# Optimization experiments

Hardware: AMD Instinct MI355X
Metric: run time of the kernel (lower is better)

Reference implementation:

```python
import jax, jax.numpy as jnp
import numpy as np

N = 20000   # nodes
E = 320000  # directed edges (before self-loops)
D = 64      # input_dim
H = 10      # GAT heads
HD = H * D  # 640
NEG_SLOPE = 0.2


def setup_inputs() -> dict:
    key = jax.random.key(0)
    ks = jax.random.split(key, 10)
    return {
        "x": jax.random.normal(ks[0], (N, D), jnp.float32),
        "W_gat": jax.random.normal(ks[1], (D, HD), jnp.float32) / np.sqrt(D).astype(np.float32),
        "att_src": jax.random.normal(ks[2], (H, D), jnp.float32) / np.sqrt(D).astype(np.float32),
        "att_dst": jax.random.normal(ks[3], (H, D), jnp.float32) / np.sqrt(D).astype(np.float32),
        "b_gat": jnp.zeros((HD,), jnp.float32),
        "W_gcn": jax.random.normal(ks[4], (HD, HD), jnp.float32) / np.sqrt(HD).astype(np.float32),
        "b_gcn": jnp.zeros((HD,), jnp.float32),
        "W1": jax.random.normal(ks[5], (2 * HD, 1500), jnp.float32) / np.sqrt(2 * HD).astype(np.float32),
        "b1": jnp.zeros((1500,), jnp.float32),
        "W2": jax.random.normal(ks[6], (1500, 10), jnp.float32) / np.sqrt(1500).astype(np.float32),
        "b2": jnp.zeros((10,), jnp.float32),
        "edge_index": jax.random.randint(ks[7], (2, E), 0, N, dtype=jnp.int64),
    }


def _forward(x, W_gat, att_src, att_dst, b_gat, W_gcn, b_gcn, W1, b1, W2, b2, edge_index):
    n = x.shape[0]
    # add self-loops (PyG default for both GATConv and GCNConv)
    loop = jnp.arange(n, dtype=edge_index.dtype)
    ei = jnp.concatenate([edge_index, jnp.stack([loop, loop])], axis=1)
    src, dst = ei[0], ei[1]

    # ---- GATConv(D -> D, heads=H, concat) ----
    xl = (x @ W_gat).reshape(n, H, D)                      # [N,H,D]
    a_src = jnp.einsum('nhd,hd->nh', xl, att_src)          # [N,H]
    a_dst = jnp.einsum('nhd,hd->nh', xl, att_dst)          # [N,H]
    alpha = jax.nn.leaky_relu(a_src[src] + a_dst[dst], NEG_SLOPE)  # [E',H]
    m = jax.ops.segment_max(alpha, dst, num_segments=n)    # segment softmax over incoming edges
    ex = jnp.exp(alpha - m[dst])
    den = jax.ops.segment_sum(ex, dst, num_segments=n)
    w = ex / (den[dst] + 1e-16)                            # [E',H]
    msg = xl[src] * w[:, :, None]                          # [E',H,D]
    x1 = jax.ops.segment_sum(msg, dst, num_segments=n).reshape(n, HD) + b_gat
    x1 = jax.nn.relu(x1)

    # ---- GCNConv(HD -> HD), symmetric norm with self-loops ----
    deg = jax.ops.segment_sum(jnp.ones(ei.shape[1], x.dtype), dst, num_segments=n)
    dinv = jnp.where(deg > 0, jax.lax.rsqrt(deg), 0.0)
    norm = dinv[src] * dinv[dst]                           # [E']
    xw = x1 @ W_gcn                                        # [N,HD]
    x2 = jax.ops.segment_sum(xw[src] * norm[:, None], dst, num_segments=n) + b_gcn
    x2 = jax.nn.relu(x2)

    # ---- global max/mean pool (batch=None -> single graph) + MLP head ----
    pooled = jnp.concatenate([x2.max(axis=0, keepdims=True),
                              x2.mean(axis=0, keepdims=True)], axis=1)  # [1, 2*HD]
    h = jax.nn.relu(pooled @ W1 + b1)
    # dropout is identity in eval mode
    return h @ W2 + b2                                     # [1, 10]


def reference(x, W_gat, att_src, att_dst, b_gat, W_gcn, b_gcn, W1, b1, W2, b2, edge_index):
    return _forward(x, W_gat, att_src, att_dst, b_gat, W_gcn, b_gcn, W1, b1, W2, b2, edge_index)
```

## Files before the change

### kernel.cpp

```cpp
#include <hip/hip_runtime.h>
#include <hip/hip_bf16.h>
#include <math.h>

#define NN 20000
#define DD 64
#define HH 10
#define HDIM 640
#define NEG 0.2f
#define H1 1500
#define BKK 128

typedef _Float16 half8 __attribute__((ext_vector_type(8)));
typedef _Float16 half4v __attribute__((ext_vector_type(4)));
typedef float f32x4 __attribute__((ext_vector_type(4)));

__global__ __launch_bounds__(256) void k_cvtB(const float* __restrict__ Wgcn,
                                              const float* __restrict__ Wg,
                                              _Float16* __restrict__ Wbt,
                                              _Float16* __restrict__ WgT)
{
    __shared__ float t[32][33];
    const int bx = blockIdx.x;
    int by = blockIdx.y;
    const float* W; _Float16* WT; int rows, cols;
    if (by < 20) { W = Wgcn; WT = Wbt; rows = HDIM; cols = HDIM; }
    else         { W = Wg;   WT = WgT; rows = DD;   cols = HDIM; by -= 20; }
    const int lx = threadIdx.x & 31, ly = threadIdx.x >> 5;
    #pragma unroll
    for (int i = ly; i < 32; i += 8)
        t[i][lx] = W[(size_t)(by * 32 + i) * cols + bx * 32 + lx];
    __syncthreads();
    #pragma unroll
    for (int j = ly; j < 32; j += 8)
        WT[(size_t)(bx * 32 + j) * rows + by * 32 + lx] = (_Float16)t[lx][j];
}

__global__ __launch_bounds__(256) void k_gemm1(
    const float* __restrict__ x, const _Float16* __restrict__ WgT,
    const float* __restrict__ att_s, const float* __restrict__ att_d,
    _Float16* __restrict__ xl, float* __restrict__ aST, float* __restrict__ aDT)
{
    __shared__ _Float16 As[128][72];
    __shared__ _Float16 Bs[64][72];
    const int tid = threadIdx.x;
    const int m0 = blockIdx.x * 128;
    const int h  = blockIdx.y;
    const int n0 = h * 64;

    {
        const int row = tid >> 1, ch = (tid & 1) * 32;
        const int gr = m0 + row;
        if (gr < NN) {
            const float* xp = &x[(size_t)gr * DD + ch];
            #pragma unroll
            for (int i = 0; i < 8; ++i) {
                const float4 v = *(const float4*)&xp[i * 4];
                half4v o = {(_Float16)v.x, (_Float16)v.y, (_Float16)v.z, (_Float16)v.w};
                *(half4v*)&As[row][ch + i * 4] = o;
            }
        } else {
            const half8 z = {0, 0, 0, 0, 0, 0, 0, 0};
            #pragma unroll
            for (int i = 0; i < 4; ++i) *(half8*)&As[row][ch + i * 8] = z;
        }
    }
    {
        const int row = tid >> 2, part = (tid & 3) * 16;
        const _Float16* wp = &WgT[(size_t)(n0 + row) * DD + part];
        *(half8*)&Bs[row][part]     = *(const half8*)&wp[0];
        *(half8*)&Bs[row][part + 8] = *(const half8*)&wp[8];
    }
    __syncthreads();

    const int lane = tid & 63, wave = tid >> 6;
    const int l15 = lane & 15, quad = lane >> 4;
    f32x4 acc[2][4];
    #pragma unroll
    for (int r = 0; r < 2; ++r)
        #pragma unroll
        for (int c = 0; c < 4; ++c) acc[r][c] = (f32x4){0.f, 0.f, 0.f, 0.f};

    #pragma unroll
    for (int ks = 0; ks < 2; ++ks) {
        const half8 a0 = *(const half8*)&As[wave * 32 + l15][ks * 32 + quad * 8];
        const half8 a1 = *(const half8*)&As[wave * 32 + 16 + l15][ks * 32 + quad * 8];
        #pragma unroll
        for (int c = 0; c < 4; ++c) {
            const half8 b = *(const half8*)&Bs[c * 16 + l15][ks * 32 + quad * 8];
            acc[0][c] = __builtin_amdgcn_mfma_f32_16x16x32_f16(a0, b, acc[0][c], 0, 0, 0);
            acc[1][c] = __builtin_amdgcn_mfma_f32_16x16x32_f16(a1, b, acc[1][c], 0, 0, 0);
        }
    }

    float asv[4], adv[4];
    #pragma unroll
    for (int c = 0; c < 4; ++c) {
        asv[c] = att_s[h * DD + c * 16 + l15];
        adv[c] = att_d[h * DD + c * 16 + l15];
    }
    #pragma unroll
    for (int r = 0; r < 2; ++r) {
        float ps[4] = {0.f, 0.f, 0.f, 0.f}, pd[4] = {0.f, 0.f, 0.f, 0.f};
        #pragma unroll
        for (int c = 0; c < 4; ++c)
            #pragma unroll
            for (int g = 0; g < 4; ++g) {
                ps[g] = fmaf(acc[r][c][g], asv[c], ps[g]);
                pd[g] = fmaf(acc[r][c][g], adv[c], pd[g]);
            }
        #pragma unroll
        for (int m = 1; m <= 8; m <<= 1)
            #pragma unroll
            for (int g = 0; g < 4; ++g) {
                ps[g] += __shfl_xor(ps[g], m);
                pd[g] += __shfl_xor(pd[g], m);
            }
        #pragma unroll
        for (int c = 0; c < 4; ++c)
            #pragma unroll
            for (int g = 0; g < 4; ++g) {
                const int row = m0 + wave * 32 + r * 16 + quad * 4 + g;
                if (row < NN)
                    xl[(size_t)row * HDIM + n0 + c * 16 + l15] = (_Float16)acc[r][c][g];
            }
        if (l15 == 0)
            #pragma unroll
            for (int g = 0; g < 4; ++g) {
                const int row = m0 + wave * 32 + r * 16 + quad * 4 + g;
                if (row < NN) {
                    aST[(size_t)h * NN + row] = ps[g];
                    aDT[(size_t)h * NN + row] = pd[g];
                }
            }
    }
}

__global__ void k_count(const int* __restrict__ ei, int E, int* __restrict__ cnt)
{
    const int e = blockIdx.x * blockDim.x + threadIdx.x;
    if (e >= E + NN) return;
    const int d = (e < E) ? ei[E + e] : (e - E);
    atomicAdd(&cnt[d], 1);
}

__global__ __launch_bounds__(1024) void k_scan(const int* __restrict__ cnt,
                                               int* __restrict__ rowptr,
                                               float* __restrict__ dinv)
{
    __shared__ int sh[1024];
    const int t = threadIdx.x;
    const int CH = 20;
    const int base = t * CH;
    int loc[CH];
    int s = 0;
    #pragma unroll
    for (int i = 0; i < CH; ++i) {
        const int idx = base + i;
        const int c = (idx < NN) ? cnt[idx] : 0;
        loc[i] = s; s += c;
    }
    sh[t] = s; __syncthreads();
    for (int off = 1; off < 1024; off <<= 1) {
        const int v = (t >= off) ? sh[t - off] : 0;
        __syncthreads();
        sh[t] += v;
        __syncthreads();
    }
    const int prev = (t == 0) ? 0 : sh[t - 1];
    #pragma unroll
    for (int i = 0; i < CH; ++i) {
        const int idx = base + i;
        if (idx < NN) {
            rowptr[idx] = prev + loc[i];
            dinv[idx]   = rsqrtf((float)cnt[idx]);
        }
    }
    if (t == 1023) rowptr[NN] = sh[1023];
}

__global__ void k_fill(const int* __restrict__ ei, int E,
                       const int* __restrict__ rowptr,
                       int* __restrict__ cursor, int* __restrict__ csr)
{
    const int e = blockIdx.x * blockDim.x + threadIdx.x;
    if (e >= E + NN) return;
    int s, d;
    if (e < E) { s = ei[e]; d = ei[E + e]; } else { s = d = e - E; }
    const int pos = atomicAdd(&cursor[d], 1);
    csr[rowptr[d] + pos] = s;
}

__device__ __forceinline__ bool slice_map3(int bid, int& s, int& m)
{
    const int r = bid & 7, k = bid >> 3;
    if (k < 625) { s = r; m = k; return true; }
    s = 8 + (r >> 2);
    m = (r & 3) * 157 + (k - 625);
    return m < 625;
}

__device__ __forceinline__ float lrexp(float a)
{
    a = (a >= 0.f) ? a : NEG * a;
    return __expf(a);
}

__global__ __launch_bounds__(256) void k_gat_gather4(
    const int* __restrict__ rowptr, const int* __restrict__ csr,
    const float* __restrict__ aST, const float* __restrict__ aDT,
    const _Float16* __restrict__ xl, const float* __restrict__ b_gat,
    _Float16* __restrict__ x1)
{
    int s, m;
    if (!slice_map3(blockIdx.x, s, m)) return;
    const int wave = threadIdx.x >> 6, lane = threadIdx.x & 63;
    const int g = lane >> 3, l = lane & 7;
    const int n = m * 32 + wave * 8 + g;
    const int col = s * 64 + l * 8;
    const float* __restrict__ as = aST + (size_t)s * NN;
    const _Float16* __restrict__ xc = xl + col;
    const float ad = aDT[(size_t)s * NN + n];

    float acc[8];
    #pragma unroll
    for (int i = 0; i < 8; ++i) acc[i] = 0.f;
    float ws = 0.f;

    const int j0 = rowptr[n], j1 = rowptr[n + 1];
    int j = j0;
    for (; j + 3 < j1; j += 4) {
        const int sA = csr[j], sB = csr[j + 1], sC = csr[j + 2], sD = csr[j + 3];
        const float wA = lrexp(as[sA] + ad);
        const float wB = lrexp(as[sB] + ad);
        const float wC = lrexp(as[sC] + ad);
        const float wD = lrexp(as[sD] + ad);
        ws += wA + wB + wC + wD;
        const half8 vA = *(const half8*)&xc[(size_t)sA * HDIM];
        const half8 vB = *(const half8*)&xc[(size_t)sB * HDIM];
        const half8 vC = *(const half8*)&xc[(size_t)sC * HDIM];
        const half8 vD = *(const half8*)&xc[(size_t)sD * HDIM];
        #pragma unroll
        for (int i = 0; i < 8; ++i) {
            acc[i] = fmaf(wA, (float)vA[i], acc[i]);
            acc[i] = fmaf(wB, (float)vB[i], acc[i]);
            acc[i] = fmaf(wC, (float)vC[i], acc[i]);
            acc[i] = fmaf(wD, (float)vD[i], acc[i]);
        }
    }
    for (; j < j1; ++j) {
        const int sA = csr[j];
        const float wA = lrexp(as[sA] + ad);
        ws += wA;
        const half8 vA = *(const half8*)&xc[(size_t)sA * HDIM];
        #pragma unroll
        for (int i = 0; i < 8; ++i) acc[i] = fmaf(wA, (float)vA[i], acc[i]);
    }

    const float rr = 1.f / (ws + 1e-16f);
    const float4 ba = *(const float4*)&b_gat[col];
    const float4 bb = *(const float4*)&b_gat[col + 4];
    const float bv[8] = {ba.x, ba.y, ba.z, ba.w, bb.x, bb.y, bb.z, bb.w};
    half8 o;
    #pragma unroll
    for (int i = 0; i < 8; ++i) {
        const float v = fmaf(acc[i], rr, bv[i]);
        o[i] = (_Float16)((v > 0.f) ? v : 0.f);
    }
    *(half8*)&x1[(size_t)n * HDIM + col] = o;
}

__global__ __launch_bounds__(256) void k_gcn_gather4(
    const int* __restrict__ rowptr, const int* __restrict__ csr,
    const float* __restrict__ dinv, const _Float16* __restrict__ x1,
    _Float16* __restrict__ t)
{
    int s, m;
    if (!slice_map3(blockIdx.x, s, m)) return;
    const int wave = threadIdx.x >> 6, lane = threadIdx.x & 63;
    const int g = lane >> 3, l = lane & 7;
    const int n = m * 32 + wave * 8 + g;
    const int col = s * 64 + l * 8;
    const _Float16* __restrict__ xc = x1 + col;
    const float dd = dinv[n];

    float acc[8];
    #pragma unroll
    for (int i = 0; i < 8; ++i) acc[i] = 0.f;

    const int j0 = rowptr[n], j1 = rowptr[n + 1];
    int j = j0;
    for (; j + 3 < j1; j += 4) {
        const int sA = csr[j], sB = csr[j + 1], sC = csr[j + 2], sD = csr[j + 3];
        const float wA = dinv[sA] * dd, wB = dinv[sB] * dd;
        const float wC = dinv[sC] * dd, wD = dinv[sD] * dd;
        const half8 vA = *(const half8*)&xc[(size_t)sA * HDIM];
        const half8 vB = *(const half8*)&xc[(size_t)sB * HDIM];
        const half8 vC = *(const half8*)&xc[(size_t)sC * HDIM];
        const half8 vD = *(const half8*)&xc[(size_t)sD * HDIM];
        #pragma unroll
        for (int i = 0; i < 8; ++i) {
            acc[i] = fmaf(wA, (float)vA[i], acc[i]);
            acc[i] = fmaf(wB, (float)vB[i], acc[i]);
            acc[i] = fmaf(wC, (float)vC[i], acc[i]);
            acc[i] = fmaf(wD, (float)vD[i], acc[i]);
        }
    }
    for (; j < j1; ++j) {
        const int sA = csr[j];
        const float wA = dinv[sA] * dd;
        const half8 vA = *(const half8*)&xc[(size_t)sA * HDIM];
        #pragma unroll
        for (int i = 0; i < 8; ++i) acc[i] = fmaf(wA, (float)vA[i], acc[i]);
    }

    half8 o;
    #pragma unroll
    for (int i = 0; i < 8; ++i) o[i] = (_Float16)acc[i];
    *(half8*)&t[(size_t)n * HDIM + col] = o;
}

__global__ __launch_bounds__(256) void k_gemm2(const _Float16* __restrict__ X,
                                               const _Float16* __restrict__ Wbt,
                                               const float* __restrict__ b_gcn,
                                               float* __restrict__ pmax,
                                               float* __restrict__ psum)
{
    __shared__ _Float16 Bs[128 * BKK];
    const int tid = threadIdx.x;
    const int lane = tid & 63, wave = tid >> 6;
    const int l15 = lane & 15, quad = lane >> 4;
    const int m0 = blockIdx.x * 128 + wave * 32;
    const int n0 = blockIdx.y * 128;
    const int l7 = l15 & 7;

    f32x4 acc[2][8];
    #pragma unroll
    for (int r = 0; r < 2; ++r)
        #pragma unroll
        for (int c = 0; c < 8; ++c) acc[r][c] = (f32x4){0.f, 0.f, 0.f, 0.f};

    const int jrow = lane >> 4;
    const int jchunk = lane & 15;

    const _Float16* a0p = &X[(size_t)(m0 + l15) * HDIM + quad * 8];
    const _Float16* a1p = a0p + (size_t)16 * HDIM;

    for (int kb = 0; kb < HDIM; kb += BKK) {
        #pragma unroll
        for (int i = 0; i < 8; ++i) {
            const int r = (wave * 8 + i) * 4 + jrow;
            const int ck = jchunk ^ (r & 7);
            const _Float16* src = &Wbt[(size_t)(n0 + r) * HDIM + kb + ck * 8];
            __builtin_amdgcn_global_load_lds(
                (const __attribute__((address_space(1))) void*)src,
                (__attribute__((address_space(3))) void*)&Bs[(size_t)(wave * 8 + i) * 512],
                16, 0, 0);
        }
        half8 a0[4], a1[4];
        #pragma unroll
        for (int ks = 0; ks < 4; ++ks) {
            a0[ks] = *(const half8*)(a0p + kb + ks * 32);
            a1[ks] = *(const half8*)(a1p + kb + ks * 32);
        }
        __syncthreads();
        #pragma unroll
        for (int ks = 0; ks < 4; ++ks) {
            #pragma unroll
            for (int c = 0; c < 8; ++c) {
                const int br = c * 16 + l15;
                const int ck = (4 * ks + quad) ^ l7;
                const half8 b = *(const half8*)&Bs[(size_t)br * BKK + ck * 8];
                acc[0][c] = __builtin_amdgcn_mfma_f32_16x16x32_f16(a0[ks], b, acc[0][c], 0, 0, 0);
                acc[1][c] = __builtin_amdgcn_mfma_f32_16x16x32_f16(a1[ks], b, acc[1][c], 0, 0, 0);
            }
        }
        __syncthreads();
    }

    float lmax[8], lsum[8];
    #pragma unroll
    for (int c = 0; c < 8; ++c) { lmax[c] = 0.f; lsum[c] = 0.f; }
    #pragma unroll
    for (int c = 0; c < 8; ++c) {
        const float bb = b_gcn[n0 + c * 16 + l15];
        #pragma unroll
        for (int r = 0; r < 2; ++r)
            #pragma unroll
            for (int g = 0; g < 4; ++g) {
                const int row = m0 + r * 16 + quad * 4 + g;
                if (row < NN) {
                    float v = acc[r][c][g] + bb;
                    v = (v > 0.f) ? v : 0.f;
                    lmax[c] = fmaxf(lmax[c], v);
                    lsum[c] += v;
                }
            }
    }
    float* redm = (float*)Bs;
    float* reds = redm + 128;
    if (tid < 128) { redm[tid] = 0.f; reds[tid] = 0.f; }
    __syncthreads();
    #pragma unroll
    for (int c = 0; c < 8; ++c) {
        const int col = c * 16 + l15;
        atomicMax((int*)&redm[col], __float_as_int(lmax[c]));
        atomicAdd(&reds[col], lsum[c]);
    }
    __syncthreads();
    if (tid < 128) {
        atomicMax((int*)&pmax[n0 + tid], __float_as_int(redm[tid]));
        atomicAdd(&psum[n0 + tid], reds[tid]);
    }
}

__global__ __launch_bounds__(256) void k_mlp1(const float* __restrict__ pmax,
                                              const float* __restrict__ psum,
                                              const float* __restrict__ W1,
                                              float* __restrict__ hacc)
{
    __shared__ float pl[80];
    const int t = threadIdx.x;
    const int i0 = blockIdx.y * 80;
    if (t < 80) {
        const int i = i0 + t;
        pl[t] = (i < HDIM) ? pmax[i] : psum[i - HDIM] * (1.0f / NN);
    }
    __syncthreads();
    const int j = blockIdx.x * 256 + t;
    if (j >= H1) return;
    float acc = 0.f;
    #pragma unroll 8
    for (int i = 0; i < 80; ++i)
        acc = fmaf(pl[i], W1[(size_t)(i0 + i) * H1 + j], acc);
    atomicAdd(&hacc[j], acc);
}

__global__ __launch_bounds__(256) void k_mlp2(const float* __restrict__ hacc,
                                              const float* __restrict__ b1,
                                              const float* __restrict__ W2,
                                              const float* __restrict__ b2,
                                              float* __restrict__ out)
{
    __shared__ float hsh[H1];
    __shared__ float red[256];
    const int t = threadIdx.x;
    for (int i = t; i < H1; i += 256) {
        const float v = hacc[i] + b1[i];
        hsh[i] = (v > 0.f) ? v : 0.f;
    }
    __syncthreads();
    float acc[10];
    #pragma unroll
    for (int k = 0; k < 10; ++k) acc[k] = 0.f;
    for (int i = t; i < H1; i += 256) {
        const float h = hsh[i];
        #pragma unroll
        for (int k = 0; k < 10; ++k) acc[k] = fmaf(h, W2[i * 10 + k], acc[k]);
    }
    for (int k = 0; k < 10; ++k) {
        red[t] = acc[k]; __syncthreads();
        for (int s2 = 128; s2 > 0; s2 >>= 1) {
            if (t < s2) red[t] += red[t + s2];
            __syncthreads();
        }
        if (t == 0) out[k] = red[0] + b2[k];
        __syncthreads();
    }
}

extern "C" void kernel_launch(void* const* d_in, const int* in_sizes, int n_in,
                              void* d_out, int out_size, void* d_ws, size_t ws_size,
                              hipStream_t stream)
{
    const float* x     = (const float*)d_in[0];
    const float* Wg    = (const float*)d_in[1];
    const float* att_s = (const float*)d_in[2];
    const float* att_d = (const float*)d_in[3];
    const float* b_gat = (const float*)d_in[4];
    const float* Wgcn  = (const float*)d_in[5];
    const float* b_gcn = (const float*)d_in[6];
    const float* W1    = (const float*)d_in[7];
    const float* b1    = (const float*)d_in[8];
    const float* W2    = (const float*)d_in[9];
    const float* b2    = (const float*)d_in[10];
    const int*   ei    = (const int*)d_in[11];
    const int E = in_sizes[11] / 2;
    const int EP = E + NN;
    float* out = (float*)d_out;

    char* wsp = (char*)d_ws;
    size_t off = 0;
    auto alc = [&](size_t b) { void* p = wsp + off; off += (b + 255) & ~(size_t)255; return p; };
    _Float16* bufA = (_Float16*)alc((size_t)NN * HDIM * 2);
    _Float16* bufB = (_Float16*)alc((size_t)NN * HDIM * 2);
    float* aST    = (float*)alc((size_t)HH * NN * 4);
    float* aDT    = (float*)alc((size_t)HH * NN * 4);
    int*   rowptr = (int*)alc((size_t)(NN + 1) * 4);
    int*   csr    = (int*)alc((size_t)EP * 4);
    float* dinv   = (float*)alc((size_t)NN * 4);
    _Float16* Wbt = (_Float16*)alc((size_t)HDIM * HDIM * 2);
    _Float16* WgT = (_Float16*)alc((size_t)HDIM * DD * 2);
    const size_t zoff = off;
    int*   cnt    = (int*)alc((size_t)NN * 4);
    int*   cursor = (int*)alc((size_t)NN * 4);
    float* pmax   = (float*)alc((size_t)HDIM * 4);
    float* psum   = (float*)alc((size_t)HDIM * 4);
    float* hacc   = (float*)alc((size_t)H1 * 4);
    const size_t zsize = off - zoff;

    hipMemsetAsync(cnt, 0, zsize, stream);

    dim3 gw(HDIM / 32, HDIM / 32 + DD / 32);
    k_cvtB<<<gw, 256, 0, stream>>>(Wgcn, Wg, Wbt, WgT);
    dim3 g1((NN + 127) / 128, HH);
    k_gemm1<<<g1, 256, 0, stream>>>(x, WgT, att_s, att_d, bufA, aST, aDT);
    k_count<<<(EP + 255) / 256, 256, 0, stream>>>(ei, E, cnt);
    k_scan<<<1, 1024, 0, stream>>>(cnt, rowptr, dinv);
    k_fill<<<(EP + 255) / 256, 256, 0, stream>>>(ei, E, rowptr, cursor, csr);
    const int GG = 6256;
    k_gat_gather4<<<GG, 256, 0, stream>>>(rowptr, csr, aST, aDT, bufA, b_gat, bufB);
    k_gcn_gather4<<<GG, 256, 0, stream>>>(rowptr, csr, dinv, bufB, bufA);
    dim3 g2((NN + 127) / 128, HDIM / 128);
    k_gemm2<<<g2, 256, 0, stream>>>(bufA, Wbt, b_gcn, pmax, psum);
    dim3 gm1(6, 16);
    k_mlp1<<<gm1, 256, 0, stream>>>(pmax, psum, W1, hacc);
    k_mlp2<<<1, 256, 0, stream>>>(hacc, b1, W2, b2, out);
}
```

Before: 324.8 us.

## Load GEMM2 B fragments directly from global and remap blocks per XCD

The second GEMM kernel stops staging the W_gcn tile in LDS through global_load_lds with barriers. Each wave now reads its B fragments straight from global memory into registers. The launch becomes a 1-D grid of 785 blocks, and block IDs are remapped so that consecutive tiles land on the same XCD, which should improve L2 reuse of X and W rows. This removes the LDS traffic and barriers, at the cost of four times more global/L2 reads for B, since each wave fetches the full tile itself.

New measurement: 372.1 us. 1.15x slower.

```diff
diff --git a/kernel.cpp b/kernel.cpp
--- a/kernel.cpp
+++ b/kernel.cpp
@@ -325,56 +325,49 @@
                                                float* __restrict__ pmax,
                                                float* __restrict__ psum)
 {
-    __shared__ _Float16 Bs[128 * BKK];
+    const int bid = blockIdx.x;
+    const int xcd = bid & 7, kk = bid >> 3;
+    const int v = (xcd == 0) ? kk : (99 + (xcd - 1) * 98 + kk);
+    const int bx = v / 5, by = v % 5;
+
     const int tid = threadIdx.x;
     const int lane = tid & 63, wave = tid >> 6;
     const int l15 = lane & 15, quad = lane >> 4;
-    const int m0 = blockIdx.x * 128 + wave * 32;
-    const int n0 = blockIdx.y * 128;
-    const int l7 = l15 & 7;
+    const int m0 = bx * 128 + wave * 32;
+    const int n0 = by * 128;
 
     f32x4 acc[2][8];
     #pragma unroll
     for (int r = 0; r < 2; ++r)
         #pragma unroll
         for (int c = 0; c < 8; ++c) acc[r][c] = (f32x4){0.f, 0.f, 0.f, 0.f};
-
-    const int jrow = lane >> 4;
-    const int jchunk = lane & 15;
 
     const _Float16* a0p = &X[(size_t)(m0 + l15) * HDIM + quad * 8];
     const _Float16* a1p = a0p + (size_t)16 * HDIM;
+    const _Float16* bp[8];
+    #pragma unroll
+    for (int c = 0; c < 8; ++c)
+        bp[c] = &Wbt[(size_t)(n0 + c * 16 + l15) * HDIM + quad * 8];
 
     for (int kb = 0; kb < HDIM; kb += BKK) {
-        #pragma unroll
-        for (int i = 0; i < 8; ++i) {
-            const int r = (wave * 8 + i) * 4 + jrow;
-            const int ck = jchunk ^ (r & 7);
-            const _Float16* src = &Wbt[(size_t)(n0 + r) * HDIM + kb + ck * 8];
-            __builtin_amdgcn_global_load_lds(
-                (const __attribute__((address_space(1))) void*)src,
-                (__attribute__((address_space(3))) void*)&Bs[(size_t)(wave * 8 + i) * 512],
-                16, 0, 0);
-        }
         half8 a0[4], a1[4];
         #pragma unroll
         for (int ks = 0; ks < 4; ++ks) {
             a0[ks] = *(const half8*)(a0p + kb + ks * 32);
             a1[ks] = *(const half8*)(a1p + kb + ks * 32);
         }
-        __syncthreads();
         #pragma unroll
         for (int ks = 0; ks < 4; ++ks) {
+            half8 b[8];
+            #pragma unroll
+            for (int c = 0; c < 8; ++c)
+                b[c] = *(const half8*)(bp[c] + kb + ks * 32);
             #pragma unroll
             for (int c = 0; c < 8; ++c) {
-                const int br = c * 16 + l15;
-                const int ck = (4 * ks + quad) ^ l7;
-                const half8 b = *(const half8*)&Bs[(size_t)br * BKK + ck * 8];
-                acc[0][c] = __builtin_amdgcn_mfma_f32_16x16x32_f16(a0[ks], b, acc[0][c], 0, 0, 0);
-                acc[1][c] = __builtin_amdgcn_mfma_f32_16x16x32_f16(a1[ks], b, acc[1][c], 0, 0, 0);
-            }
-        }
-        __syncthreads();
+                acc[0][c] = __builtin_amdgcn_mfma_f32_16x16x32_f16(a0[ks], b[c], acc[0][c], 0, 0, 0);
+                acc[1][c] = __builtin_amdgcn_mfma_f32_16x16x32_f16(a1[ks], b[c], acc[1][c], 0, 0, 0);
+            }
+        }
     }
 
     float lmax[8], lsum[8];
@@ -389,15 +382,15 @@
             for (int g = 0; g < 4; ++g) {
                 const int row = m0 + r * 16 + quad * 4 + g;
                 if (row < NN) {
-                    float v = acc[r][c][g] + bb;
-                    v = (v > 0.f) ? v : 0.f;
-                    lmax[c] = fmaxf(lmax[c], v);
-                    lsum[c] += v;
+                    float val = acc[r][c][g] + bb;
+                    val = (val > 0.f) ? val : 0.f;
+                    lmax[c] = fmaxf(lmax[c], val);
+                    lsum[c] += val;
                 }
             }
     }
-    float* redm = (float*)Bs;
-    float* reds = redm + 128;
+    __shared__ float redm[128];
+    __shared__ float reds[128];
     if (tid < 128) { redm[tid] = 0.f; reds[tid] = 0.f; }
     __syncthreads();
     #pragma unroll
@@ -520,8 +513,7 @@
     const int GG = 6256;
     k_gat_gather4<<<GG, 256, 0, stream>>>(rowptr, csr, aST, aDT, bufA, b_gat, bufB);
     k_gcn_gather4<<<GG, 256, 0, stream>>>(rowptr, csr, dinv, bufB, bufA);
-    dim3 g2((NN + 127) / 128, HDIM / 128);
-    k_gemm2<<<g2, 256, 0, stream>>>(bufA, Wbt, b_gcn, pmax, psum);
+    k_gemm2<<<785, 256, 0, stream>>>(bufA, Wbt, b_gcn, pmax, psum);
     dim3 gm1(6, 16);
     k_mlp1<<<gm1, 256, 0, stream>>>(pmax, psum, W1, hacc);
     k_mlp2<<<1, 256, 0, stream>>>(hacc, b1, W2, b2, out);
```

## Double-buffer B tiles in GCN GEMM and remap blocks for XCD locality

Applied to the files above, without the earlier changes.

Gives the second GEMM's weight tile two LDS buffers and prefetches the next K-slice with global_load_lds while MFMAs run on the current one. Explicit vmcnt waits and raw s_barrier replace the two __syncthreads per iteration. The 2D grid becomes a 1D grid of 800 blocks, remapped so the 8 consecutive block ids (round-robined across XCDs) take different row strips and each XCD works on its own set of strips across all N tiles, improving L2 reuse of the A rows. This doubles LDS use to 64KB per block, which may reduce occupancy, and relies on hand-counted vmcnt values being correct.

Result: faster. 317.4 us (-2.3%).

```diff
diff --git a/kernel.cpp b/kernel.cpp
--- a/kernel.cpp
+++ b/kernel.cpp
@@ -325,57 +325,75 @@
                                                float* __restrict__ pmax,
                                                float* __restrict__ psum)
 {
-    __shared__ _Float16 Bs[128 * BKK];
+    __shared__ _Float16 Bs[2][128 * BKK];
+    const int bid = blockIdx.x;
+    const int r = bid & 7, q = bid >> 3;
+    const int strip = (q / 5) * 8 + r;
+    const int nt = q % 5;
+    if (strip >= 157) return;
+
     const int tid = threadIdx.x;
     const int lane = tid & 63, wave = tid >> 6;
     const int l15 = lane & 15, quad = lane >> 4;
-    const int m0 = blockIdx.x * 128 + wave * 32;
-    const int n0 = blockIdx.y * 128;
+    const int m0 = strip * 128 + wave * 32;
+    const int n0 = nt * 128;
     const int l7 = l15 & 7;
+    const int jrow = lane >> 4, jchunk = lane & 15;
 
     f32x4 acc[2][8];
     #pragma unroll
-    for (int r = 0; r < 2; ++r)
-        #pragma unroll
-        for (int c = 0; c < 8; ++c) acc[r][c] = (f32x4){0.f, 0.f, 0.f, 0.f};
-
-    const int jrow = lane >> 4;
-    const int jchunk = lane & 15;
+    for (int rr = 0; rr < 2; ++rr)
+        #pragma unroll
+        for (int c = 0; c < 8; ++c) acc[rr][c] = (f32x4){0.f, 0.f, 0.f, 0.f};
 
     const _Float16* a0p = &X[(size_t)(m0 + l15) * HDIM + quad * 8];
     const _Float16* a1p = a0p + (size_t)16 * HDIM;
 
-    for (int kb = 0; kb < HDIM; kb += BKK) {
-        #pragma unroll
-        for (int i = 0; i < 8; ++i) {
-            const int r = (wave * 8 + i) * 4 + jrow;
-            const int ck = jchunk ^ (r & 7);
-            const _Float16* src = &Wbt[(size_t)(n0 + r) * HDIM + kb + ck * 8];
-            __builtin_amdgcn_global_load_lds(
-                (const __attribute__((address_space(1))) void*)src,
-                (__attribute__((address_space(3))) void*)&Bs[(size_t)(wave * 8 + i) * 512],
-                16, 0, 0);
-        }
+#define STAGE2(buf, kb)                                                          \
+    {                                                                            \
+        _Pragma("unroll")                                                        \
+        for (int i = 0; i < 8; ++i) {                                            \
+            const int rw = (wave * 8 + i) * 4 + jrow;                            \
+            const int ck = jchunk ^ (rw & 7);                                    \
+            const _Float16* src = &Wbt[(size_t)(n0 + rw) * HDIM + (kb) + ck * 8];\
+            __builtin_amdgcn_global_load_lds(                                    \
+                (const __attribute__((address_space(1))) void*)src,              \
+                (__attribute__((address_space(3))) void*)&Bs[buf][(size_t)(wave * 8 + i) * 512], \
+                16, 0, 0);                                                       \
+        }                                                                        \
+    }
+
+    STAGE2(0, 0);
+    for (int it = 0; it < 5; ++it) {
+        const int kb = it * BKK;
         half8 a0[4], a1[4];
         #pragma unroll
         for (int ks = 0; ks < 4; ++ks) {
             a0[ks] = *(const half8*)(a0p + kb + ks * 32);
             a1[ks] = *(const half8*)(a1p + kb + ks * 32);
         }
-        __syncthreads();
+        if (it < 4) {
+            STAGE2((it + 1) & 1, kb + BKK);
+            asm volatile("s_waitcnt vmcnt(8)" ::: "memory");
+        } else {
+            asm volatile("s_waitcnt vmcnt(0)" ::: "memory");
+        }
+        __builtin_amdgcn_s_barrier();
+        const _Float16* Bsc = Bs[it & 1];
         #pragma unroll
         for (int ks = 0; ks < 4; ++ks) {
             #pragma unroll
             for (int c = 0; c < 8; ++c) {
                 const int br = c * 16 + l15;
                 const int ck = (4 * ks + quad) ^ l7;
-                const half8 b = *(const half8*)&Bs[(size_t)br * BKK + ck * 8];
+                const half8 b = *(const half8*)&Bsc[(size_t)br * BKK + ck * 8];
                 acc[0][c] = __builtin_amdgcn_mfma_f32_16x16x32_f16(a0[ks], b, acc[0][c], 0, 0, 0);
                 acc[1][c] = __builtin_amdgcn_mfma_f32_16x16x32_f16(a1[ks], b, acc[1][c], 0, 0, 0);
             }
         }
-        __syncthreads();
-    }
+        __builtin_amdgcn_s_barrier();
+    }
+#undef STAGE2
 
     float lmax[8], lsum[8];
     #pragma unroll
@@ -384,12 +402,12 @@
     for (int c = 0; c < 8; ++c) {
         const float bb = b_gcn[n0 + c * 16 + l15];
         #pragma unroll
-        for (int r = 0; r < 2; ++r)
+        for (int rr = 0; rr < 2; ++rr)
             #pragma unroll
             for (int g = 0; g < 4; ++g) {
-                const int row = m0 + r * 16 + quad * 4 + g;
+                const int row = m0 + rr * 16 + quad * 4 + g;
                 if (row < NN) {
-                    float v = acc[r][c][g] + bb;
+                    float v = acc[rr][c][g] + bb;
                     v = (v > 0.f) ? v : 0.f;
                     lmax[c] = fmaxf(lmax[c], v);
                     lsum[c] += v;
@@ -520,8 +538,7 @@
     const int GG = 6256;
     k_gat_gather4<<<GG, 256, 0, stream>>>(rowptr, csr, aST, aDT, bufA, b_gat, bufB);
     k_gcn_gather4<<<GG, 256, 0, stream>>>(rowptr, csr, dinv, bufB, bufA);
-    dim3 g2((NN + 127) / 128, HDIM / 128);
-    k_gemm2<<<g2, 256, 0, stream>>>(bufA, Wbt, b_gcn, pmax, psum);
+    k_gemm2<<<800, 256, 0, stream>>>(bufA, Wbt, b_gcn, pmax, psum);
     dim3 gm1(6, 16);
     k_mlp1<<<gm1, 256, 0, stream>>>(pmax, psum, W1, hacc);
     k_mlp2<<<1, 256, 0, stream>>>(hacc, b1, W2, b2, out);
```
